# Performance work log

Measured on AMD Instinct MI355X. Metric: run time of the kernel, lower is better.

Reference implementation:

```python
import jax, jax.numpy as jnp
import numpy as np

M, N = 8192, 8192
BITS = 3
BETA1, BETA2 = 16, 16
NNZ_PER_ROW = 32


def setup_inputs() -> dict:
    key = jax.random.key(0)
    ks = jax.random.split(key, 10)
    tm, tn = M // BETA1, N // BETA2
    nnz = M * NNZ_PER_ROW
    x = jax.random.normal(ks[0], (1, 10, N), dtype=jnp.float32)
    # quantized weight codes and first-order quantized scale/zero codes (3-bit)
    W = jax.random.randint(ks[1], (M, N), 0, 2 ** BITS, dtype=jnp.int32)
    W_s = jax.random.randint(ks[2], (M, tn), 0, 2 ** BITS, dtype=jnp.int32)
    W_z = jax.random.randint(ks[3], (M, tn), 0, 2 ** BITS, dtype=jnp.int32)
    # second-order (per-tile) float scale/zero for the quantized scales/zeros
    W_s_s = jax.random.uniform(ks[4], (tm, tn), jnp.float32, 0.01, 0.1)
    W_s_z = jax.random.uniform(ks[5], (tm, tn), jnp.float32, 0.0, 1.0)
    W_z_s = jax.random.uniform(ks[6], (tm, tn), jnp.float32, 0.01, 0.1)
    W_z_z = jax.random.uniform(ks[7], (tm, tn), jnp.float32, 0.0, 1.0)
    # CSR outliers: fixed 32 nnz per row
    row_offsets = jnp.arange(M + 1, dtype=jnp.int32) * NNZ_PER_ROW
    col_ids = jax.random.randint(ks[8], (nnz,), 0, N, dtype=jnp.int32)
    values = jax.random.normal(ks[9], (nnz,), dtype=jnp.float32)
    return dict(x=x, W=W, W_s=W_s, W_z=W_z, W_s_s=W_s_s, W_s_z=W_s_z,
                W_z_s=W_z_s, W_z_z=W_z_z, row_offsets=row_offsets,
                col_ids=col_ids, values=values)


def _dequantize(W, W_s, W_z, W_s_s, W_s_z, W_z_s, W_z_z):
    m, n = W.shape
    tm, tn = W_s_s.shape
    beta1, beta2 = m // tm, n // tn
    # two-level dequant: first-order scale/zero are themselves quantized per tile
    s = (W_s.astype(jnp.float32).reshape(tm, beta1, tn) - W_s_z[:, None, :]) * W_s_s[:, None, :]
    z = (W_z.astype(jnp.float32).reshape(tm, beta1, tn) - W_z_z[:, None, :]) * W_z_s[:, None, :]
    s = s.reshape(m, tn)  # (m, n/beta2)
    z = z.reshape(m, tn)
    w = (W.astype(jnp.float32).reshape(m, tn, beta2) - z[:, :, None]) * s[:, :, None]
    return w.reshape(m, n)


def reference(x, W, W_s, W_z, W_s_s, W_s_z, W_z_s, W_z_z, row_offsets, col_ids, values):
    Wd = _dequantize(W, W_s, W_z, W_s_s, W_s_z, W_z_s, W_z_z)  # (m, n)
    m = Wd.shape[0]
    b, l, n = x.shape
    xf = x.reshape(b * l, n)
    # dense quantized matmul: y = x @ Wd^T
    y = jnp.einsum('bn,mn->bm', xf, Wd)
    # CSR sparse outlier correction
    nnz = values.shape[0]
    rows = jnp.repeat(jnp.arange(m, dtype=jnp.int32), jnp.diff(row_offsets),
                      total_repeat_length=nnz)
    contrib = values[:, None] * xf[:, col_ids].T  # (nnz, B)
    y = y + jax.ops.segment_sum(contrib, rows, num_segments=m).T
    return y.reshape(b, l, m)
```

## Files before the change

### kernel.cpp

```cpp
#include <hip/hip_runtime.h>
#include <hip/hip_bf16.h>


constexpr int M_DIM = 8192;
constexpr int N_DIM = 8192;
constexpr int TN    = 512;
constexpr int BQ    = 10;
constexpr int KSPLIT = 16;
constexpr int KRANGE = N_DIM / KSPLIT;
constexpr int KITERS = KRANGE / 32;
constexpr int RPB    = 64;
constexpr int GPB    = KRANGE / 16;

typedef float  f32x4  __attribute__((ext_vector_type(4)));
typedef int    i32x4  __attribute__((ext_vector_type(4)));
typedef short  bf16x8 __attribute__((ext_vector_type(8)));

__device__ inline int pkbf(float a, float b) {
    __hip_bfloat162 h = __float22bfloat162_rn(float2{a, b});
    int r;
    __builtin_memcpy(&r, &h, 4);
    return r;
}

__global__ __launch_bounds__(256, 4)
void spqr_mfma(const float* __restrict__ x,
               const int*   __restrict__ W,
               const int*   __restrict__ Ws,
               const int*   __restrict__ Wz,
               const float* __restrict__ Wss,
               const float* __restrict__ Wsz,
               const float* __restrict__ Wzs,
               const float* __restrict__ Wzz,
               float*       __restrict__ pws)
{
    __shared__ int   ldsA[KITERS * 64 * 4];
    __shared__ float ldsS[RPB * 33];
    __shared__ float ldsZ[RPB * 33];

    const int t   = threadIdx.x;
    const int m0b = blockIdx.x * RPB;
    const int ks  = blockIdx.y;
    const int k0  = ks * KRANGE;
    const int g0  = k0 >> 4;

    for (int idx = t; idx < KITERS * 64; idx += 256) {
        const int kk = idx >> 6, l = idx & 63;
        const int b = l & 15, koff = (kk << 5) + ((l >> 4) << 3);
        int out[4] = {0, 0, 0, 0};
        if (b < BQ) {
            const float* xp = x + b * N_DIM + k0 + koff;
            f32x4 lo = *reinterpret_cast<const f32x4*>(xp);
            f32x4 hi = *reinterpret_cast<const f32x4*>(xp + 4);
            out[0] = pkbf(lo.x, lo.y);
            out[1] = pkbf(lo.z, lo.w);
            out[2] = pkbf(hi.x, hi.y);
            out[3] = pkbf(hi.z, hi.w);
        }
        *reinterpret_cast<i32x4*>(&ldsA[idx * 4]) = *reinterpret_cast<i32x4*>(out);
    }

    for (int idx = t; idx < RPB * GPB; idx += 256) {
        const int rl = idx >> 5;
        const int gl = idx & 31;
        const int m = m0b + rl, g = g0 + gl;
        const int tix = (m >> 4) * TN + g;
        ldsS[rl * 33 + gl] = ((float)Ws[m * TN + g] - Wsz[tix]) * Wss[tix];
        ldsZ[rl * 33 + gl] = ((float)Wz[m * TN + g] - Wzz[tix]) * Wzs[tix];
    }
    __syncthreads();

    const int wv = t >> 6, l = t & 63;
    const int lrow = l & 15;
    const int lk   = l >> 4;
    const int m0   = m0b + (wv << 4);
    const int* wp  = W + (size_t)(m0 + lrow) * N_DIM + k0 + (lk << 3);
    const int szrow = (wv << 4) + lrow;
    const int szk   = lk >> 1;

    f32x4 acc = {0.f, 0.f, 0.f, 0.f};
    i32x4 cbufL[4], cbufH[4];

    #pragma unroll
    for (int p = 0; p < 3; ++p) {
        cbufL[p] = *reinterpret_cast<const i32x4*>(wp + p * 32);
        cbufH[p] = *reinterpret_cast<const i32x4*>(wp + p * 32 + 4);
    }

    #pragma unroll 4
    for (int kk = 0; kk < KITERS; ++kk) {
        if (kk + 3 < KITERS) {
            cbufL[(kk + 3) & 3] = *reinterpret_cast<const i32x4*>(wp + (kk + 3) * 32);
            cbufH[(kk + 3) & 3] = *reinterpret_cast<const i32x4*>(wp + (kk + 3) * 32 + 4);
        }
        const i32x4 a4 = *reinterpret_cast<const i32x4*>(&ldsA[(kk * 64 + l) * 4]);
        const float s   = ldsS[szrow * 33 + kk * 2 + szk];
        const float z   = ldsZ[szrow * 33 + kk * 2 + szk];
        const float nzs = -z * s;
        const i32x4 cl = cbufL[kk & 3], ch = cbufH[kk & 3];
        int bw[4];
        bw[0] = pkbf(fmaf((float)cl.x, s, nzs), fmaf((float)cl.y, s, nzs));
        bw[1] = pkbf(fmaf((float)cl.z, s, nzs), fmaf((float)cl.w, s, nzs));
        bw[2] = pkbf(fmaf((float)ch.x, s, nzs), fmaf((float)ch.y, s, nzs));
        bw[3] = pkbf(fmaf((float)ch.z, s, nzs), fmaf((float)ch.w, s, nzs));
        const bf16x8 af = __builtin_bit_cast(bf16x8, a4);
        i32x4 bwv = *reinterpret_cast<i32x4*>(bw);
        const bf16x8 bf = __builtin_bit_cast(bf16x8, bwv);
        acc = __builtin_amdgcn_mfma_f32_16x16x32_bf16(af, bf, acc, 0, 0, 0);
    }

    float* pb = pws + (size_t)ks * (BQ * N_DIM) + (m0 + lrow);
    #pragma unroll
    for (int j = 0; j < 4; ++j) {
        const int b = (lk << 2) + j;
        if (b < BQ) pb[(size_t)b * N_DIM] = acc[j];
    }
}

__global__ __launch_bounds__(256, 4)
void spqr_reduce(const float* __restrict__ x,
                 const int*   __restrict__ row_offsets,
                 const int*   __restrict__ col_ids,
                 const float* __restrict__ values,
                 const float* __restrict__ pws,
                 float*       __restrict__ y)
{
    __shared__ float lsp[8][BQ];
    const int t  = threadIdx.x;
    const int m0 = blockIdx.x * 8;

    {
        const int r = t >> 5, j = t & 31;
        const int m = m0 + r;
        const int base = row_offsets[m];
        const int cnt  = row_offsets[m + 1] - base;
        float c[BQ];
        #pragma unroll
        for (int b = 0; b < BQ; ++b) c[b] = 0.f;
        for (int jj = j; jj < cnt; jj += 32) {
            const int   col = col_ids[base + jj];
            const float v   = values[base + jj];
            #pragma unroll
            for (int b = 0; b < BQ; ++b)
                c[b] = fmaf(v, x[b * N_DIM + col], c[b]);
        }
        #pragma unroll
        for (int b = 0; b < BQ; ++b) {
            float v = c[b];
            for (int off = 16; off > 0; off >>= 1)
                v += __shfl_xor(v, off, 32);
            c[b] = v;
        }
        if (j == 0) {
            #pragma unroll
            for (int b = 0; b < BQ; ++b) lsp[r][b] = c[b];
        }
    }
    __syncthreads();

    if (t < 8 * BQ) {
        const int ml = t / BQ, b = t % BQ;
        const int m = m0 + ml;
        float v = lsp[ml][b];
        const float* pp = pws + (size_t)b * N_DIM + m;
        #pragma unroll
        for (int ksp = 0; ksp < KSPLIT; ++ksp)
            v += pp[(size_t)ksp * (BQ * N_DIM)];
        y[(size_t)b * M_DIM + m] = v;
    }
}

extern "C" void kernel_launch(void* const* d_in, const int* in_sizes, int n_in,
                              void* d_out, int out_size, void* d_ws, size_t ws_size,
                              hipStream_t stream)
{
    const float* x    = (const float*)d_in[0];
    const int*   W    = (const int*)  d_in[1];
    const int*   Ws   = (const int*)  d_in[2];
    const int*   Wz   = (const int*)  d_in[3];
    const float* Wss  = (const float*)d_in[4];
    const float* Wsz  = (const float*)d_in[5];
    const float* Wzs  = (const float*)d_in[6];
    const float* Wzz  = (const float*)d_in[7];
    const int*   roff = (const int*)  d_in[8];
    const int*   cids = (const int*)  d_in[9];
    const float* vals = (const float*)d_in[10];
    float* yout = (float*)d_out;
    float* pws  = (float*)d_ws;

    dim3 grid1(M_DIM / RPB, KSPLIT);
    spqr_mfma<<<grid1, dim3(256), 0, stream>>>(x, W, Ws, Wz, Wss, Wsz, Wzs, Wzz, pws);

    dim3 grid2(M_DIM / 8);
    spqr_reduce<<<grid2, dim3(256), 0, stream>>>(x, roff, cids, vals, pws, yout);
}
```

Baseline: 81.34 us.

## Move sparse outlier pass into MFMA grid, pack scale/zero, deepen prefetch

Adds an extra grid slice to the MFMA kernel that computes the CSR outlier contributions into a seventeenth partial buffer, so the sparse gather overlaps with the dense work. The reduce kernel becomes a flat sum over the partial buffers. Scale and negated zero*scale are packed as two bf16 values in one LDS word, which saves LDS space and a multiply per iteration but lowers the precision of the scale/zero terms. The weight prefetch depth goes from 3 to 6 with full unrolling, which increases register pressure.

```diff
diff --git a/kernel.cpp b/kernel.cpp
--- a/kernel.cpp
+++ b/kernel.cpp
@@ -11,6 +11,7 @@
 constexpr int KITERS = KRANGE / 32;
 constexpr int RPB    = 64;
 constexpr int GPB    = KRANGE / 16;
+constexpr int DEPTH  = 6;
 
 typedef float  f32x4  __attribute__((ext_vector_type(4)));
 typedef int    i32x4  __attribute__((ext_vector_type(4)));
@@ -32,17 +33,54 @@
                const float* __restrict__ Wsz,
                const float* __restrict__ Wzs,
                const float* __restrict__ Wzz,
+               const int*   __restrict__ row_offsets,
+               const int*   __restrict__ col_ids,
+               const float* __restrict__ values,
                float*       __restrict__ pws)
 {
-    __shared__ int   ldsA[KITERS * 64 * 4];
-    __shared__ float ldsS[RPB * 33];
-    __shared__ float ldsZ[RPB * 33];
-
     const int t   = threadIdx.x;
     const int m0b = blockIdx.x * RPB;
     const int ks  = blockIdx.y;
-    const int k0  = ks * KRANGE;
-    const int g0  = k0 >> 4;
+
+    if (ks == KSPLIT) {
+        const int r8 = t >> 5;
+        const int j  = t & 31;
+        float* pb = pws + (size_t)KSPLIT * (BQ * N_DIM);
+        for (int rr = r8; rr < RPB; rr += 8) {
+            const int m = m0b + rr;
+            const int base = row_offsets[m];
+            const int cnt  = row_offsets[m + 1] - base;
+            float c[BQ];
+            #pragma unroll
+            for (int b = 0; b < BQ; ++b) c[b] = 0.f;
+            for (int jj = j; jj < cnt; jj += 32) {
+                const int   col = col_ids[base + jj];
+                const float v   = values[base + jj];
+                #pragma unroll
+                for (int b = 0; b < BQ; ++b)
+                    c[b] = fmaf(v, x[b * N_DIM + col], c[b]);
+            }
+            #pragma unroll
+            for (int b = 0; b < BQ; ++b) {
+                float v = c[b];
+                for (int off = 16; off > 0; off >>= 1)
+                    v += __shfl_xor(v, off, 32);
+                c[b] = v;
+            }
+            if (j == 0) {
+                #pragma unroll
+                for (int b = 0; b < BQ; ++b)
+                    pb[(size_t)b * N_DIM + m] = c[b];
+            }
+        }
+        return;
+    }
+
+    __shared__ int ldsA[KITERS * 64 * 4];
+    __shared__ int ldsSZ[RPB * 33];
+
+    const int k0 = ks * KRANGE;
+    const int g0 = k0 >> 4;
 
     for (int idx = t; idx < KITERS * 64; idx += 256) {
         const int kk = idx >> 6, l = idx & 63;
@@ -65,8 +103,9 @@
         const int gl = idx & 31;
         const int m = m0b + rl, g = g0 + gl;
         const int tix = (m >> 4) * TN + g;
-        ldsS[rl * 33 + gl] = ((float)Ws[m * TN + g] - Wsz[tix]) * Wss[tix];
-        ldsZ[rl * 33 + gl] = ((float)Wz[m * TN + g] - Wzz[tix]) * Wzs[tix];
+        const float s = ((float)Ws[m * TN + g] - Wsz[tix]) * Wss[tix];
+        const float z = ((float)Wz[m * TN + g] - Wzz[tix]) * Wzs[tix];
+        ldsSZ[rl * 33 + gl] = pkbf(s, -z * s);
     }
     __syncthreads();
 
@@ -79,25 +118,27 @@
     const int szk   = lk >> 1;
 
     f32x4 acc = {0.f, 0.f, 0.f, 0.f};
-    i32x4 cbufL[4], cbufH[4];
-
-    #pragma unroll
-    for (int p = 0; p < 3; ++p) {
+    i32x4 cbufL[DEPTH], cbufH[DEPTH];
+
+    #pragma unroll
+    for (int p = 0; p < DEPTH; ++p) {
         cbufL[p] = *reinterpret_cast<const i32x4*>(wp + p * 32);
         cbufH[p] = *reinterpret_cast<const i32x4*>(wp + p * 32 + 4);
     }
 
-    #pragma unroll 4
+    #pragma unroll
     for (int kk = 0; kk < KITERS; ++kk) {
-        if (kk + 3 < KITERS) {
-            cbufL[(kk + 3) & 3] = *reinterpret_cast<const i32x4*>(wp + (kk + 3) * 32);
-            cbufH[(kk + 3) & 3] = *reinterpret_cast<const i32x4*>(wp + (kk + 3) * 32 + 4);
+        const i32x4 cl = cbufL[kk % DEPTH], ch = cbufH[kk % DEPTH];
+        if (kk + DEPTH < KITERS) {
+            cbufL[kk % DEPTH] =
+                *reinterpret_cast<const i32x4*>(wp + (kk + DEPTH) * 32);
+            cbufH[kk % DEPTH] =
+                *reinterpret_cast<const i32x4*>(wp + (kk + DEPTH) * 32 + 4);
         }
         const i32x4 a4 = *reinterpret_cast<const i32x4*>(&ldsA[(kk * 64 + l) * 4]);
-        const float s   = ldsS[szrow * 33 + kk * 2 + szk];
-        const float z   = ldsZ[szrow * 33 + kk * 2 + szk];
-        const float nzs = -z * s;
-        const i32x4 cl = cbufL[kk & 3], ch = cbufH[kk & 3];
+        const int spk = ldsSZ[szrow * 33 + kk * 2 + szk];
+        const float s   = __uint_as_float((unsigned)spk << 16);
+        const float nzs = __uint_as_float((unsigned)spk & 0xffff0000u);
         int bw[4];
         bw[0] = pkbf(fmaf((float)cl.x, s, nzs), fmaf((float)cl.y, s, nzs));
         bw[1] = pkbf(fmaf((float)cl.z, s, nzs), fmaf((float)cl.w, s, nzs));
@@ -118,56 +159,19 @@
 }
 
 __global__ __launch_bounds__(256, 4)
-void spqr_reduce(const float* __restrict__ x,
-                 const int*   __restrict__ row_offsets,
-                 const int*   __restrict__ col_ids,
-                 const float* __restrict__ values,
-                 const float* __restrict__ pws,
+void spqr_reduce(const float* __restrict__ pws,
                  float*       __restrict__ y)
 {
-    __shared__ float lsp[8][BQ];
-    const int t  = threadIdx.x;
-    const int m0 = blockIdx.x * 8;
-
-    {
-        const int r = t >> 5, j = t & 31;
-        const int m = m0 + r;
-        const int base = row_offsets[m];
-        const int cnt  = row_offsets[m + 1] - base;
-        float c[BQ];
-        #pragma unroll
-        for (int b = 0; b < BQ; ++b) c[b] = 0.f;
-        for (int jj = j; jj < cnt; jj += 32) {
-            const int   col = col_ids[base + jj];
-            const float v   = values[base + jj];
-            #pragma unroll
-            for (int b = 0; b < BQ; ++b)
-                c[b] = fmaf(v, x[b * N_DIM + col], c[b]);
-        }
-        #pragma unroll
-        for (int b = 0; b < BQ; ++b) {
-            float v = c[b];
-            for (int off = 16; off > 0; off >>= 1)
-                v += __shfl_xor(v, off, 32);
-            c[b] = v;
-        }
-        if (j == 0) {
-            #pragma unroll
-            for (int b = 0; b < BQ; ++b) lsp[r][b] = c[b];
-        }
-    }
-    __syncthreads();
-
-    if (t < 8 * BQ) {
-        const int ml = t / BQ, b = t % BQ;
-        const int m = m0 + ml;
-        float v = lsp[ml][b];
-        const float* pp = pws + (size_t)b * N_DIM + m;
-        #pragma unroll
-        for (int ksp = 0; ksp < KSPLIT; ++ksp)
-            v += pp[(size_t)ksp * (BQ * N_DIM)];
-        y[(size_t)b * M_DIM + m] = v;
-    }
+    const int gid = blockIdx.x * 256 + threadIdx.x;
+    if (gid >= BQ * M_DIM) return;
+    const int b = gid / M_DIM;
+    const int m = gid - b * M_DIM;
+    const float* pp = pws + (size_t)b * N_DIM + m;
+    float v = 0.f;
+    #pragma unroll
+    for (int ksp = 0; ksp < KSPLIT + 1; ++ksp)
+        v += pp[(size_t)ksp * (BQ * N_DIM)];
+    y[(size_t)b * M_DIM + m] = v;
 }
 
 extern "C" void kernel_launch(void* const* d_in, const int* in_sizes, int n_in,
@@ -188,9 +192,10 @@
     float* yout = (float*)d_out;
     float* pws  = (float*)d_ws;
 
-    dim3 grid1(M_DIM / RPB, KSPLIT);
-    spqr_mfma<<<grid1, dim3(256), 0, stream>>>(x, W, Ws, Wz, Wss, Wsz, Wzs, Wzz, pws);
-
-    dim3 grid2(M_DIM / 8);
-    spqr_reduce<<<grid2, dim3(256), 0, stream>>>(x, roff, cids, vals, pws, yout);
-}
+    dim3 grid1(M_DIM / RPB, KSPLIT + 1);
+    spqr_mfma<<<grid1, dim3(256), 0, stream>>>(x, W, Ws, Wz, Wss, Wsz, Wzs, Wzz,
+                                               roff, cids, vals, pws);
+
+    dim3 grid2((BQ * M_DIM + 255) / 256);
+    spqr_reduce<<<grid2, dim3(256), 0, stream>>>(pws, yout);
+}
```

New measurement: 82.77 us. About the same (+1.8%).
